# Performance work log

Measured on AMD Instinct MI355X. Metric: run time of the kernel, lower is better.

The kernel has to match this reference:

```python
import jax, jax.numpy as jnp
import numpy as np

DIM = 64      # channels C
RES = 128     # input_resolution (H = W)
WIN = 16      # ka_win_num
KS = 3        # kernel_size
WS = RES // int(np.sqrt(WIN))   # window_size = 32
NW = RES // WS                  # 4 windows per side
B = 4


def _dw_conv(x, w, groups):
    # depthwise conv, stride 1, pad 1; x:(N,G,H,W), w:(G,1,k,k)
    return jax.lax.conv_general_dilated(
        x, w, window_strides=(1, 1), padding=((1, 1), (1, 1)),
        feature_group_count=groups,
        dimension_numbers=('NCHW', 'OIHW', 'NCHW'))


def setup_inputs() -> dict:
    key = jax.random.key(0)
    ks = jax.random.split(key, 12)
    f = lambda k, shape: jax.random.normal(k, shape, jnp.float32) * 0.02
    return dict(
        x=jax.random.normal(ks[0], (B, RES * RES, DIM), jnp.float32),
        # ConvLayer1 depthwise params: torch uses plain randn init
        conv1_w=jax.random.normal(ks[1], (WIN * DIM, 1, KS, KS), jnp.float32),
        dc_w=f(ks[2], (WIN, DIM)), dc_b=f(ks[3], (WIN,)),
        l1_w=f(ks[4], (4 * WIN, WIN)), l1_b=f(ks[5], (4 * WIN,)),
        l2_w=f(ks[6], (WIN, 4 * WIN)), l2_b=f(ks[7], (WIN,)),
        gk_w=f(ks[8], (WIN,)), gk_b=f(ks[9], ()),
        fus_w=f(ks[10], (DIM, (WIN + 1) * DIM)), fus_b=f(ks[11], (DIM,)),
    )


def reference(x, conv1_w, dc_w, dc_b, l1_w, l1_b, l2_w, l2_b,
              gk_w, gk_b, fus_w, fus_b):
    b = x.shape[0]
    # pad_feature_map is a no-op here (RES % WS == 0)
    xw = (x.reshape(b, NW, WS, NW, WS, DIM)
           .transpose(0, 1, 3, 5, 2, 4)
           .reshape(b, WIN * DIM, WS, WS))
    # convlayer1: depthwise 3x3 per (window, channel)
    win_conv = _dw_conv(xw, conv1_w, WIN * DIM)
    # WinKernel_Reweight: pool -> grouped 1x1 -> 1x1 -> GELU -> 1x1 -> sigmoid
    pooled = win_conv.mean(axis=(2, 3)).reshape(b, WIN, DIM)
    w = jnp.einsum('bwc,wc->bw', pooled, dc_w) + dc_b
    w = jax.nn.gelu(w @ l1_w.T + l1_b, approximate=False)   # torch GELU is exact
    w = jax.nn.sigmoid(w @ l2_w.T + l2_b)
    # reweight per-window depthwise kernels
    base = conv1_w.reshape(WIN, DIM, KS, KS)
    kernels = w[:, :, None, None, None] * base[None]
    # global kernel: 1x1 conv over window axis
    gk = jnp.einsum('w,bwdij->bdij', gk_w, kernels) + gk_b  # (B, DIM, KS, KS)
    all_k = jnp.concatenate([kernels, gk[:, None]], axis=1)
    all_k = all_k.reshape(b * (WIN + 1) * DIM, 1, KS, KS)
    # apply per-sample dynamic depthwise kernels on the full-res map
    xi = x.reshape(b, RES, RES, DIM).transpose(0, 3, 1, 2)  # (B, C, H, W)
    xr = jnp.tile(xi, (1, WIN + 1, 1, 1)).reshape(1, b * (WIN + 1) * DIM, RES, RES)
    y = _dw_conv(xr, all_k, b * (WIN + 1) * DIM)
    y = y.reshape(b, (WIN + 1) * DIM, RES, RES)
    # fusion 1x1 conv
    y = jnp.einsum('bchw,oc->bohw', y, fus_w) + fus_b[None, :, None, None]
    return y.transpose(0, 2, 3, 1).reshape(b, RES * RES, DIM)
```

## Files before the change

kernel.cpp:

```cpp
#include <hip/hip_runtime.h>
#include <math.h>

#define BB   4
#define DIM  64
#define RES  128
#define WIN  16
#define WS   32

typedef __attribute__((ext_vector_type(8))) short bf16x8;
typedef __attribute__((ext_vector_type(4))) float f32x4;

static __device__ __forceinline__ unsigned short bf16_rne(float f) {
  unsigned int u = __float_as_uint(f);
  u += 0x7FFFu + ((u >> 16) & 1u);
  return (unsigned short)(u >> 16);
}
static __device__ __forceinline__ float bf16_f(unsigned short h) {
  return __uint_as_float(((unsigned int)h) << 16);
}

__global__ __launch_bounds__(1024) void k_pooled(
    const float* __restrict__ x, const float* __restrict__ conv1_w,
    float* __restrict__ pooled)
{
  const int blk = blockIdx.x;
  const int b = blk >> 4, w = blk & 15;
  const int wy = w >> 2, wx = w & 3;
  const int c = threadIdx.x & 63, rg = threadIdx.x >> 6;
  const float* xb = x + (size_t)b * RES * RES * DIM + c;

  float T = 0.f, R0 = 0.f, RL = 0.f, C0 = 0.f, CL = 0.f;
  for (int ii = 0; ii < 2; ++ii) {
    const int i  = rg * 2 + ii;
    const int gr = wy * WS + i;
    const float* xr = xb + (size_t)(gr * RES + wx * WS) * DIM;
    float rs = 0.f, v0 = 0.f, vL = 0.f;
#pragma unroll 8
    for (int j = 0; j < 32; ++j) {
      float v = xr[(size_t)j * DIM];
      rs += v;
      if (j == 0)  v0 = v;
      if (j == 31) vL = v;
    }
    T += rs; C0 += v0; CL += vL;
    if (i == 0)  R0 += rs;
    if (i == 31) RL += rs;
  }

  __shared__ float part[16][5][64];
  part[rg][0][c] = T;  part[rg][1][c] = R0; part[rg][2][c] = RL;
  part[rg][3][c] = C0; part[rg][4][c] = CL;
  __syncthreads();

  if (threadIdx.x < 64) {
    const int cc = threadIdx.x;
    float t = 0, r0 = 0, rl = 0, c0 = 0, cl = 0;
#pragma unroll
    for (int q = 0; q < 16; ++q) {
      t += part[q][0][cc]; r0 += part[q][1][cc]; rl += part[q][2][cc];
      c0 += part[q][3][cc]; cl += part[q][4][cc];
    }
    const float* xc = x + (size_t)b * RES * RES * DIM + cc;
    const size_t b00 = (size_t)(wy * WS * RES + wx * WS) * DIM;
    const float x00 = xc[b00];
    const float x0L = xc[b00 + 31 * DIM];
    const float xL0 = xc[b00 + (size_t)31 * RES * DIM];
    const float xLL = xc[b00 + (size_t)31 * RES * DIM + 31 * DIM];

    const float* bw = conv1_w + (size_t)(w * DIM + cc) * 9;
    float p = 0.f;
#pragma unroll
    for (int ky = 0; ky < 3; ++ky) {
#pragma unroll
      for (int kx = 0; kx < 3; ++kx) {
        const int dy = ky - 1, dx = kx - 1;
        float S = t;
        if (dy == 1)  S -= r0;
        if (dy == -1) S -= rl;
        if (dx == 1)  S -= c0;
        if (dx == -1) S -= cl;
        if (dy == 1 && dx == 1)   S += x00;
        if (dy == 1 && dx == -1)  S += x0L;
        if (dy == -1 && dx == 1)  S += xL0;
        if (dy == -1 && dx == -1) S += xLL;
        p += bw[ky * 3 + kx] * S;
      }
    }
    pooled[blk * 64 + cc] = p * (1.0f / 1024.0f);
  }
}

__global__ __launch_bounds__(576) void k_keff(
    const float* __restrict__ pooled, const float* __restrict__ conv1_w,
    const float* __restrict__ dc_w, const float* __restrict__ dc_b,
    const float* __restrict__ l1_w, const float* __restrict__ l1_b,
    const float* __restrict__ l2_w, const float* __restrict__ l2_b,
    const float* __restrict__ gk_w, const float* __restrict__ gk_b,
    const float* __restrict__ fus_w,
    unsigned short* __restrict__ kT_hi, unsigned short* __restrict__ kT_lo)
{
  const int b = blockIdx.x >> 6, o = blockIdx.x & 63;
  const int tid = threadIdx.x;
  __shared__ float w1s[16], hs[64], w2s[16], gkws[16];

  if (tid < 16) {
    float s = dc_b[tid];
    const float* p  = pooled + b * 1024 + tid * 64;
    const float* dw = dc_w + tid * 64;
    for (int cc = 0; cc < 64; ++cc) s += p[cc] * dw[cc];
    w1s[tid] = s;
    gkws[tid] = gk_w[tid];
  }
  __syncthreads();
  if (tid < 64) {
    float s = l1_b[tid];
    for (int g = 0; g < 16; ++g) s += w1s[g] * l1_w[tid * 16 + g];
    hs[tid] = 0.5f * s * (1.0f + erff(s * 0.70710678118654752f));
  }
  __syncthreads();
  if (tid < 16) {
    float s = l2_b[tid];
    for (int j = 0; j < 64; ++j) s += hs[j] * l2_w[tid * 64 + j];
    w2s[tid] = 1.0f / (1.0f + expf(-s));
  }
  __syncthreads();

  const int tap = tid >> 6, c = tid & 63;
  const float f1 = fus_w[o * 1088 + 1024 + c];
  float acc = gk_b[0] * f1;
#pragma unroll
  for (int g = 0; g < 16; ++g) {
    acc += w2s[g] * conv1_w[(size_t)(g * 64 + c) * 9 + tap] *
           (fus_w[o * 1088 + g * 64 + c] + gkws[g] * f1);
  }
  const unsigned short h = bf16_rne(acc);
  const unsigned short lo = bf16_rne(acc - bf16_f(h));
  const size_t kidx = (size_t)(b * 64 + o) * 576 + tid;
  kT_hi[kidx] = h;
  kT_lo[kidx] = lo;
}

__global__ __launch_bounds__(256, 2) void k_conv(
    const float* __restrict__ x,
    const unsigned short* __restrict__ kT_hi,
    const unsigned short* __restrict__ kT_lo,
    const float* __restrict__ fus_b, float* __restrict__ out)
{
  const int bid = blockIdx.x;
  const int b = bid >> 7, row = bid & 127;
  const int tid = threadIdx.x;
  const int l = tid & 63, wv = tid >> 6;
  const int l16 = l & 15, lq = l >> 4;

  __shared__ unsigned short xs_hi[3][130][40];
  __shared__ unsigned short xs_lo[3][130][40];

  f32x4 acc[2][4];
#pragma unroll
  for (int mf = 0; mf < 2; ++mf)
#pragma unroll
    for (int nf = 0; nf < 4; ++nf) acc[mf][nf] = (f32x4){0.f, 0.f, 0.f, 0.f};

  const float* xb = x + (size_t)b * RES * RES * DIM;
  const unsigned short* khB = kT_hi + (size_t)b * 64 * 576;
  const unsigned short* klB = kT_lo + (size_t)b * 64 * 576;

  for (int ch = 0; ch < 2; ++ch) {
    const int c0 = ch * 32;
    for (int i = tid; i < 3 * 130 * 8; i += 256) {
      const int rr  = i / (130 * 8);
      const int rem = i - rr * (130 * 8);
      const int cs  = rem >> 3;
      const int c4  = rem & 7;
      const int col = cs - 1;
      const int grow = row - 1 + rr;
      float4 v = make_float4(0.f, 0.f, 0.f, 0.f);
      if (grow >= 0 && grow < RES && col >= 0 && col < RES)
        v = *(const float4*)(xb + (size_t)(grow * RES + col) * DIM + c0 + c4 * 4);
      const unsigned short h0 = bf16_rne(v.x), h1 = bf16_rne(v.y),
                           h2 = bf16_rne(v.z), h3 = bf16_rne(v.w);
      const unsigned short q0 = bf16_rne(v.x - bf16_f(h0)),
                           q1 = bf16_rne(v.y - bf16_f(h1)),
                           q2 = bf16_rne(v.z - bf16_f(h2)),
                           q3 = bf16_rne(v.w - bf16_f(h3));
      *(ushort4*)&xs_hi[rr][cs][c4 * 4] = make_ushort4(h0, h1, h2, h3);
      *(ushort4*)&xs_lo[rr][cs][c4 * 4] = make_ushort4(q0, q1, q2, q3);
    }
    __syncthreads();

    const int pcol = wv * 32 + l16;
#pragma unroll
    for (int tap = 0; tap < 9; ++tap) {
      const int dy = tap / 3 - 1, dx = tap % 3 - 1;
      const int kb = tap * 64 + c0 + lq * 8;
      bf16x8 Bh[4], Bl[4];
#pragma unroll
      for (int nf = 0; nf < 4; ++nf) {
        const size_t ko = (size_t)(nf * 16 + l16) * 576 + kb;
        Bh[nf] = *(const bf16x8*)(khB + ko);
        Bl[nf] = *(const bf16x8*)(klB + ko);
      }
      bf16x8 Ah[2], Al[2];
#pragma unroll
      for (int mf = 0; mf < 2; ++mf) {
        const int cs = 1 + pcol + mf * 16 + dx;
        Ah[mf] = *(const bf16x8*)&xs_hi[dy + 1][cs][lq * 8];
        Al[mf] = *(const bf16x8*)&xs_lo[dy + 1][cs][lq * 8];
      }
#pragma unroll
      for (int mf = 0; mf < 2; ++mf)
#pragma unroll
        for (int nf = 0; nf < 4; ++nf) {
          acc[mf][nf] = __builtin_amdgcn_mfma_f32_16x16x32_bf16(
              Ah[mf], Bh[nf], acc[mf][nf], 0, 0, 0);
          acc[mf][nf] = __builtin_amdgcn_mfma_f32_16x16x32_bf16(
              Ah[mf], Bl[nf], acc[mf][nf], 0, 0, 0);
          acc[mf][nf] = __builtin_amdgcn_mfma_f32_16x16x32_bf16(
              Al[mf], Bh[nf], acc[mf][nf], 0, 0, 0);
        }
    }
    __syncthreads();
  }

  float fb[4];
#pragma unroll
  for (int nf = 0; nf < 4; ++nf) fb[nf] = fus_b[nf * 16 + l16];
  const size_t pbase = (size_t)b * RES * RES + (size_t)row * RES;
#pragma unroll
  for (int mf = 0; mf < 2; ++mf) {
    const int pc = wv * 32 + mf * 16 + lq * 4;
#pragma unroll
    for (int r4 = 0; r4 < 4; ++r4) {
      const size_t po = (pbase + pc + r4) * DIM;
#pragma unroll
      for (int nf = 0; nf < 4; ++nf)
        out[po + nf * 16 + l16] = acc[mf][nf][r4] + fb[nf];
    }
  }
}

extern "C" void kernel_launch(void* const* d_in, const int* in_sizes, int n_in,
                              void* d_out, int out_size, void* d_ws, size_t ws_size,
                              hipStream_t stream) {
  const float* x       = (const float*)d_in[0];
  const float* conv1_w = (const float*)d_in[1];
  const float* dc_w    = (const float*)d_in[2];
  const float* dc_b    = (const float*)d_in[3];
  const float* l1_w    = (const float*)d_in[4];
  const float* l1_b    = (const float*)d_in[5];
  const float* l2_w    = (const float*)d_in[6];
  const float* l2_b    = (const float*)d_in[7];
  const float* gk_w    = (const float*)d_in[8];
  const float* gk_b    = (const float*)d_in[9];
  const float* fus_w   = (const float*)d_in[10];
  const float* fus_b   = (const float*)d_in[11];
  float* out = (float*)d_out;

  float* pooled = (float*)d_ws;
  unsigned short* kT_hi = (unsigned short*)((char*)d_ws + 16384);
  unsigned short* kT_lo = kT_hi + (size_t)BB * 64 * 576;

  hipLaunchKernelGGL(k_pooled, dim3(BB * WIN), dim3(1024), 0, stream,
                     x, conv1_w, pooled);
  hipLaunchKernelGGL(k_keff, dim3(BB * 64), dim3(576), 0, stream,
                     pooled, conv1_w, dc_w, dc_b, l1_w, l1_b, l2_w, l2_b,
                     gk_w, gk_b, fus_w, kT_hi, kT_lo);
  hipLaunchKernelGGL(k_conv, dim3(BB * RES), dim3(256), 0, stream,
                     x, kT_hi, kT_lo, fus_b, out);
}
```

Measured before the change: 143.7 us.

## Split conv blocks into half-row tiles and give each wave an output-channel slice

The conv kernel now launches two blocks per image row, each covering 64 columns, with a smaller shared-memory halo tile. Each wave now owns 16 output channels across all 64 pixels instead of 32 pixels across all 64 channels, so it loads a single B fragment per tap. Launch bounds go up to 4 blocks per CU. The aim is more blocks in flight, better occupancy and less per-wave kernel-weight register traffic. The cost is more redundant halo loading and fp32-to-bf16 conversion of x, plus narrower strided output stores.

```diff
diff --git a/kernel.cpp b/kernel.cpp
--- a/kernel.cpp
+++ b/kernel.cpp
@@ -140,26 +140,27 @@
   kT_lo[kidx] = lo;
 }
 
-__global__ __launch_bounds__(256, 2) void k_conv(
+__global__ __launch_bounds__(256, 4) void k_conv(
     const float* __restrict__ x,
     const unsigned short* __restrict__ kT_hi,
     const unsigned short* __restrict__ kT_lo,
     const float* __restrict__ fus_b, float* __restrict__ out)
 {
   const int bid = blockIdx.x;
-  const int b = bid >> 7, row = bid & 127;
+  const int b = bid >> 8;
+  const int rem = bid & 255;
+  const int row = rem >> 1;
+  const int colbase = (rem & 1) * 64;
   const int tid = threadIdx.x;
   const int l = tid & 63, wv = tid >> 6;
   const int l16 = l & 15, lq = l >> 4;
 
-  __shared__ unsigned short xs_hi[3][130][40];
-  __shared__ unsigned short xs_lo[3][130][40];
-
-  f32x4 acc[2][4];
-#pragma unroll
-  for (int mf = 0; mf < 2; ++mf)
-#pragma unroll
-    for (int nf = 0; nf < 4; ++nf) acc[mf][nf] = (f32x4){0.f, 0.f, 0.f, 0.f};
+  __shared__ unsigned short xs_hi[3][68][40];
+  __shared__ unsigned short xs_lo[3][68][40];
+
+  f32x4 acc[4];
+#pragma unroll
+  for (int mf = 0; mf < 4; ++mf) acc[mf] = (f32x4){0.f, 0.f, 0.f, 0.f};
 
   const float* xb = x + (size_t)b * RES * RES * DIM;
   const unsigned short* khB = kT_hi + (size_t)b * 64 * 576;
@@ -167,12 +168,12 @@
 
   for (int ch = 0; ch < 2; ++ch) {
     const int c0 = ch * 32;
-    for (int i = tid; i < 3 * 130 * 8; i += 256) {
-      const int rr  = i / (130 * 8);
-      const int rem = i - rr * (130 * 8);
-      const int cs  = rem >> 3;
-      const int c4  = rem & 7;
-      const int col = cs - 1;
+    for (int i = tid; i < 3 * 66 * 8; i += 256) {
+      const int rr  = i / (66 * 8);
+      const int rem2 = i - rr * (66 * 8);
+      const int cs  = rem2 >> 3;
+      const int c4  = rem2 & 7;
+      const int col = colbase + cs - 1;
       const int grow = row - 1 + rr;
       float4 v = make_float4(0.f, 0.f, 0.f, 0.f);
       if (grow >= 0 && grow < RES && col >= 0 && col < RES)
@@ -188,53 +189,34 @@
     }
     __syncthreads();
 
-    const int pcol = wv * 32 + l16;
 #pragma unroll
     for (int tap = 0; tap < 9; ++tap) {
       const int dy = tap / 3 - 1, dx = tap % 3 - 1;
       const int kb = tap * 64 + c0 + lq * 8;
-      bf16x8 Bh[4], Bl[4];
-#pragma unroll
-      for (int nf = 0; nf < 4; ++nf) {
-        const size_t ko = (size_t)(nf * 16 + l16) * 576 + kb;
-        Bh[nf] = *(const bf16x8*)(khB + ko);
-        Bl[nf] = *(const bf16x8*)(klB + ko);
+      const size_t ko = (size_t)(wv * 16 + l16) * 576 + kb;
+      const bf16x8 Bh = *(const bf16x8*)(khB + ko);
+      const bf16x8 Bl = *(const bf16x8*)(klB + ko);
+#pragma unroll
+      for (int mf = 0; mf < 4; ++mf) {
+        const int cs = 1 + mf * 16 + l16 + dx;
+        const bf16x8 Ah = *(const bf16x8*)&xs_hi[dy + 1][cs][lq * 8];
+        const bf16x8 Al = *(const bf16x8*)&xs_lo[dy + 1][cs][lq * 8];
+        acc[mf] = __builtin_amdgcn_mfma_f32_16x16x32_bf16(Ah, Bh, acc[mf], 0, 0, 0);
+        acc[mf] = __builtin_amdgcn_mfma_f32_16x16x32_bf16(Ah, Bl, acc[mf], 0, 0, 0);
+        acc[mf] = __builtin_amdgcn_mfma_f32_16x16x32_bf16(Al, Bh, acc[mf], 0, 0, 0);
       }
-      bf16x8 Ah[2], Al[2];
-#pragma unroll
-      for (int mf = 0; mf < 2; ++mf) {
-        const int cs = 1 + pcol + mf * 16 + dx;
-        Ah[mf] = *(const bf16x8*)&xs_hi[dy + 1][cs][lq * 8];
-        Al[mf] = *(const bf16x8*)&xs_lo[dy + 1][cs][lq * 8];
-      }
-#pragma unroll
-      for (int mf = 0; mf < 2; ++mf)
-#pragma unroll
-        for (int nf = 0; nf < 4; ++nf) {
-          acc[mf][nf] = __builtin_amdgcn_mfma_f32_16x16x32_bf16(
-              Ah[mf], Bh[nf], acc[mf][nf], 0, 0, 0);
-          acc[mf][nf] = __builtin_amdgcn_mfma_f32_16x16x32_bf16(
-              Ah[mf], Bl[nf], acc[mf][nf], 0, 0, 0);
-          acc[mf][nf] = __builtin_amdgcn_mfma_f32_16x16x32_bf16(
-              Al[mf], Bh[nf], acc[mf][nf], 0, 0, 0);
-        }
     }
     __syncthreads();
   }
 
-  float fb[4];
-#pragma unroll
-  for (int nf = 0; nf < 4; ++nf) fb[nf] = fus_b[nf * 16 + l16];
-  const size_t pbase = (size_t)b * RES * RES + (size_t)row * RES;
-#pragma unroll
-  for (int mf = 0; mf < 2; ++mf) {
-    const int pc = wv * 32 + mf * 16 + lq * 4;
+  const float fb = fus_b[wv * 16 + l16];
+  const size_t pbase = (size_t)b * RES * RES + (size_t)row * RES + colbase;
+#pragma unroll
+  for (int mf = 0; mf < 4; ++mf) {
+    const int pc = mf * 16 + lq * 4;
 #pragma unroll
     for (int r4 = 0; r4 < 4; ++r4) {
-      const size_t po = (pbase + pc + r4) * DIM;
-#pragma unroll
-      for (int nf = 0; nf < 4; ++nf)
-        out[po + nf * 16 + l16] = acc[mf][nf][r4] + fb[nf];
+      out[(pbase + pc + r4) * DIM + wv * 16 + l16] = acc[mf][r4] + fb;
     }
   }
 }
@@ -265,6 +247,6 @@
   hipLaunchKernelGGL(k_keff, dim3(BB * 64), dim3(576), 0, stream,
                      pooled, conv1_w, dc_w, dc_b, l1_w, l1_b, l2_w, l2_b,
                      gk_w, gk_b, fus_w, kT_hi, kT_lo);
-  hipLaunchKernelGGL(k_conv, dim3(BB * RES), dim3(256), 0, stream,
+  hipLaunchKernelGGL(k_conv, dim3(BB * RES * 2), dim3(256), 0, stream,
                      x, kT_hi, kT_lo, fus_b, out);
 }
```

Measured after the change: 123.2 us. 14.3% less time.
